# Kernel tuning notes

Measured on AMD Instinct MI355X. Metric: run time of the kernel, lower is better.

The kernel has to match this reference:

```python
import jax, jax.numpy as jnp
import numpy as np

N = 100000   # nodes
E = 1600000  # edges
F = 128      # in = out features
BN_EPS = 1e-5


def setup_inputs() -> dict:
    key = jax.random.key(0)
    ks = jax.random.split(key, 20)
    s = 1.0 / np.sqrt(F)
    inp = {
        "x": jax.random.normal(ks[0], (N, F), dtype=jnp.float32),
        "edge_index": jax.random.randint(ks[1], (2, E), 0, N, dtype=jnp.int64),
        "edge_type": jax.random.randint(ks[2], (E,), 0, 2, dtype=jnp.int64),
        # self-loop linear
        "w_sl": jax.random.normal(ks[3], (F, F), dtype=jnp.float32) * s,
        "b_sl": jnp.zeros((F,), dtype=jnp.float32),
        # GIN MLP for relation 0 (edge_type==0)
        "w1_n": jax.random.normal(ks[4], (F, F), dtype=jnp.float32) * s,
        "b1_n": jnp.zeros((F,), dtype=jnp.float32),
        "gamma_n": jnp.ones((F,), dtype=jnp.float32),
        "beta_n": jnp.zeros((F,), dtype=jnp.float32),
        "w2_n": jax.random.normal(ks[5], (F, F), dtype=jnp.float32) * s,
        "b2_n": jnp.zeros((F,), dtype=jnp.float32),
        # GIN MLP for relation 1 (edge_type==1)
        "w1_d": jax.random.normal(ks[6], (F, F), dtype=jnp.float32) * s,
        "b1_d": jnp.zeros((F,), dtype=jnp.float32),
        "gamma_d": jnp.ones((F,), dtype=jnp.float32),
        "beta_d": jnp.zeros((F,), dtype=jnp.float32),
        "w2_d": jax.random.normal(ks[7], (F, F), dtype=jnp.float32) * s,
        "b2_d": jnp.zeros((F,), dtype=jnp.float32),
        # gate linear: 3F -> F
        "w_gat": jax.random.normal(ks[8], (F, 3 * F), dtype=jnp.float32) * (1.0 / np.sqrt(3 * F)),
        "b_gat": jnp.zeros((F,), dtype=jnp.float32),
    }
    return inp


def _gin_branch(x, src, dst, mask, w1, b1, gamma, beta, w2, b2):
    # masked gather-scatter: equivalent to selecting edge columns with edge_type==r
    msg = x[src] * mask[:, None]                         # [E, F]
    agg = jax.ops.segment_sum(msg, dst, num_segments=N)  # [N, F]
    h = agg + x                                          # (1 + eps)*x with eps=0
    h = h @ w1.T + b1
    # BatchNorm1d, training-mode batch statistics (biased variance)
    mu = jnp.mean(h, axis=0)
    var = jnp.var(h, axis=0)
    h = gamma * (h - mu) * jax.lax.rsqrt(var + BN_EPS) + beta
    h = jax.nn.relu(h)
    return h @ w2.T + b2


def reference(x, edge_index, edge_type, w_sl, b_sl,
              w1_n, b1_n, gamma_n, beta_n, w2_n, b2_n,
              w1_d, b1_d, gamma_d, beta_d, w2_d, b2_d,
              w_gat, b_gat):
    src, dst = edge_index[0], edge_index[1]
    mask_n = (edge_type == 0).astype(x.dtype)
    mask_d = (edge_type == 1).astype(x.dtype)

    x_new_x = x @ w_sl.T + b_sl
    x_new_n = _gin_branch(x, src, dst, mask_n, w1_n, b1_n, gamma_n, beta_n, w2_n, b2_n)
    x_new_d = _gin_branch(x, src, dst, mask_d, w1_d, b1_d, gamma_d, beta_d, w2_d, b2_d)

    cat = jnp.concatenate((x_new_x, x_new_n, x_new_d), axis=1)   # [N, 3F]
    gat_raw = jax.nn.softmax(cat @ w_gat.T + b_gat, axis=-1)     # [N, F]
    gat = jnp.cumsum(gat_raw, axis=-1)
    out = (x_new_x + x_new_n) * (1.0 - gat) + (x_new_x + x_new_n + jnp.flip(x_new_d, axis=1)) * gat
    return out
```

## Files before the change

kernel.cpp:

```cpp
#include <hip/hip_runtime.h>
#include <stdint.h>

#define FF 128
#define MFMA __builtin_amdgcn_mfma_f32_16x16x32_bf16

typedef __attribute__((ext_vector_type(8))) short bf8_t;
typedef __attribute__((ext_vector_type(4))) float f4_t;
typedef __attribute__((ext_vector_type(8))) uint16_t us8_t;

__device__ __forceinline__ uint16_t f2bf(float f) {
  union { float f; uint32_t u; } v; v.f = f;
  return (uint16_t)((v.u + 0x7fffu + ((v.u >> 16) & 1u)) >> 16);
}
__device__ __forceinline__ float bf2f(uint16_t h) {
  union { uint32_t u; float f; } v; v.u = ((uint32_t)h) << 16;
  return v.f;
}

#define STAGE_W(Wp, rsb, cb)                                                   \
  do {                                                                         \
    uint4 tmp_[8];                                                             \
    _Pragma("unroll") for (int j_ = 0; j_ < 8; ++j_) {                         \
      int k_ = j_ * 4 + w;                                                     \
      int r_ = ((k_ & 1) << 6) + lane;                                         \
      int c_ = k_ >> 1;                                                        \
      tmp_[j_] = *(const uint4*)((const char*)(Wp) + (size_t)r_ * (rsb) +      \
                                 (cb) + c_ * 16);                              \
    }                                                                          \
    _Pragma("unroll") for (int j_ = 0; j_ < 8; ++j_) {                         \
      int k_ = j_ * 4 + w;                                                     \
      *(uint4*)((char*)wlds + k_ * 1024 + lane * 16) = tmp_[j_];               \
    }                                                                          \
  } while (0)

__global__ __launch_bounds__(256) void cvt_w_k(
    const float* __restrict__ wsl, const float* __restrict__ w1n,
    const float* __restrict__ w2n, const float* __restrict__ w1d,
    const float* __restrict__ w2d, const float* __restrict__ wgat,
    uint16_t* __restrict__ o) {
  int i = blockIdx.x * 256 + threadIdx.x;
  const int NW = 5 * 16384;
  if (i >= NW + 49152) return;
  float v;
  if (i < NW) {
    int wsel = i >> 14, j = i & 16383;
    const float* p = (wsel == 0) ? wsl : (wsel == 1) ? w1n : (wsel == 2) ? w2n
                     : (wsel == 3) ? w1d : w2d;
    v = p[j];
  } else {
    v = wgat[i - NW];
  }
  o[i] = f2bf(v);
}

__global__ __launch_bounds__(256) void cvt_x_k(const float* __restrict__ x,
                                               uint16_t* __restrict__ xb, int n4) {
  int i = blockIdx.x * 256 + threadIdx.x;
  if (i >= n4) return;
  float4 v = ((const float4*)x)[i];
  uint2 o;
  o.x = ((uint32_t)f2bf(v.y) << 16) | f2bf(v.x);
  o.y = ((uint32_t)f2bf(v.w) << 16) | f2bf(v.z);
  ((uint2*)xb)[i] = o;
}

__global__ __launch_bounds__(256) void hist_k(const int* __restrict__ dst,
                                              const int* __restrict__ ety,
                                              int* __restrict__ hist, int E) {
  int i = blockIdx.x * 256 + threadIdx.x;
  if (i < E) atomicAdd(&hist[(dst[i] << 1) | ety[i]], 1);
}

__global__ __launch_bounds__(256) void scan1_k(const int* __restrict__ hist,
                                               int* __restrict__ off,
                                               int* __restrict__ bsum, int nbins) {
  int i = blockIdx.x * 256 + threadIdx.x;
  int v = (i < nbins) ? hist[i] : 0;
  int lane = threadIdx.x & 63, w = threadIdx.x >> 6;
  int s = v;
#pragma unroll
  for (int d = 1; d < 64; d <<= 1) {
    int o = __shfl_up(s, (unsigned)d, 64);
    if (lane >= d) s += o;
  }
  __shared__ int wsum[4];
  if (lane == 63) wsum[w] = s;
  __syncthreads();
  int add = 0;
  for (int k = 0; k < w; ++k) add += wsum[k];
  s += add;
  if (i < nbins) off[i] = s - v;
  if (threadIdx.x == 255) bsum[blockIdx.x] = s;
}

__global__ __launch_bounds__(1024) void scan2_k(int* __restrict__ bsum, int nb) {
  int t = threadIdx.x;
  int v = (t < nb) ? bsum[t] : 0;
  int lane = t & 63, w = t >> 6;
  int s = v;
#pragma unroll
  for (int d = 1; d < 64; d <<= 1) {
    int o = __shfl_up(s, (unsigned)d, 64);
    if (lane >= d) s += o;
  }
  __shared__ int ws[16];
  if (lane == 63) ws[w] = s;
  __syncthreads();
  int add = 0;
  for (int k = 0; k < w; ++k) add += ws[k];
  s += add;
  if (t < nb) bsum[t] = s - v;
}

__global__ __launch_bounds__(256) void scan3_k(int* __restrict__ off,
                                               int* __restrict__ cur,
                                               const int* __restrict__ bsum,
                                               int nbins, int E) {
  int i = blockIdx.x * 256 + threadIdx.x;
  if (i < nbins) {
    int v = off[i] + bsum[blockIdx.x];
    off[i] = v;
    cur[i] = v;
  }
  if (i == nbins) off[i] = E;
}

__global__ __launch_bounds__(256) void sctidx_k(const int* __restrict__ src,
                                                const int* __restrict__ dst,
                                                const int* __restrict__ ety,
                                                int* __restrict__ cur,
                                                int* __restrict__ ssrc, int E) {
  int i = blockIdx.x * 256 + threadIdx.x;
  if (i < E) {
    int pos = atomicAdd(&cur[(dst[i] << 1) | ety[i]], 1);
    ssrc[pos] = src[i];
  }
}

__global__ __launch_bounds__(256) void agg_k(const int* __restrict__ off,
                                             const int* __restrict__ ssrc,
                                             const uint16_t* __restrict__ xb,
                                             const float* __restrict__ x,
                                             uint16_t* __restrict__ xanb,
                                             uint16_t* __restrict__ xadb, int nbins) {
  int wid = (blockIdx.x * 256 + threadIdx.x) >> 6;
  int lane = threadIdx.x & 63;
  if (wid >= nbins) return;
  int e = off[wid], end = off[wid + 1];
  float ax = 0.f, ay = 0.f, bx = 0.f, by = 0.f;
  for (; e + 7 < end; e += 8) {
    uint32_t v0 = ((const uint32_t*)(xb + (size_t)ssrc[e] * FF))[lane];
    uint32_t v1 = ((const uint32_t*)(xb + (size_t)ssrc[e + 1] * FF))[lane];
    uint32_t v2 = ((const uint32_t*)(xb + (size_t)ssrc[e + 2] * FF))[lane];
    uint32_t v3 = ((const uint32_t*)(xb + (size_t)ssrc[e + 3] * FF))[lane];
    uint32_t v4 = ((const uint32_t*)(xb + (size_t)ssrc[e + 4] * FF))[lane];
    uint32_t v5 = ((const uint32_t*)(xb + (size_t)ssrc[e + 5] * FF))[lane];
    uint32_t v6 = ((const uint32_t*)(xb + (size_t)ssrc[e + 6] * FF))[lane];
    uint32_t v7 = ((const uint32_t*)(xb + (size_t)ssrc[e + 7] * FF))[lane];
    ax += bf2f((uint16_t)(v0 & 0xffffu)) + bf2f((uint16_t)(v2 & 0xffffu)) +
          bf2f((uint16_t)(v4 & 0xffffu)) + bf2f((uint16_t)(v6 & 0xffffu));
    ay += bf2f((uint16_t)(v0 >> 16)) + bf2f((uint16_t)(v2 >> 16)) +
          bf2f((uint16_t)(v4 >> 16)) + bf2f((uint16_t)(v6 >> 16));
    bx += bf2f((uint16_t)(v1 & 0xffffu)) + bf2f((uint16_t)(v3 & 0xffffu)) +
          bf2f((uint16_t)(v5 & 0xffffu)) + bf2f((uint16_t)(v7 & 0xffffu));
    by += bf2f((uint16_t)(v1 >> 16)) + bf2f((uint16_t)(v3 >> 16)) +
          bf2f((uint16_t)(v5 >> 16)) + bf2f((uint16_t)(v7 >> 16));
  }
  for (; e + 1 < end; e += 2) {
    uint32_t v0 = ((const uint32_t*)(xb + (size_t)ssrc[e] * FF))[lane];
    uint32_t v1 = ((const uint32_t*)(xb + (size_t)ssrc[e + 1] * FF))[lane];
    ax += bf2f((uint16_t)(v0 & 0xffffu));
    ay += bf2f((uint16_t)(v0 >> 16));
    bx += bf2f((uint16_t)(v1 & 0xffffu));
    by += bf2f((uint16_t)(v1 >> 16));
  }
  if (e < end) {
    uint32_t v0 = ((const uint32_t*)(xb + (size_t)ssrc[e] * FF))[lane];
    ax += bf2f((uint16_t)(v0 & 0xffffu));
    ay += bf2f((uint16_t)(v0 >> 16));
  }
  ax += bx;
  ay += by;
  int n = wid >> 1;
  float2 xo = ((const float2*)(x + (size_t)n * FF))[lane];
  ax += xo.x;
  ay += xo.y;
  uint32_t o = ((uint32_t)f2bf(ay) << 16) | f2bf(ax);
  uint16_t* dstp = (wid & 1) ? xadb : xanb;
  ((uint32_t*)(dstp + (size_t)n * FF))[lane] = o;
}

__global__ __launch_bounds__(256) void gemm1_k(
    const uint16_t* __restrict__ xanb, const uint16_t* __restrict__ xadb,
    const uint16_t* __restrict__ wbf, const float* __restrict__ b1n,
    const float* __restrict__ b1d, uint16_t* __restrict__ h1n,
    uint16_t* __restrict__ h1d, float* __restrict__ gstats, int N) {
  __shared__ __align__(16) uint16_t wlds[16384];
  __shared__ float sstat[4][4][128];
  const int tid = threadIdx.x;
  const int lane = tid & 63, w = tid >> 6;
  const int lr = lane & 15, lg = lane >> 4;
  const int rowbase = blockIdx.x * 128 + w * 32;
  const int arow0 = min(rowbase + lr, N - 1);
  const int arow1 = min(rowbase + 16 + lr, N - 1);

  f4_t acc[2][8];
  const f4_t zz = {0.f, 0.f, 0.f, 0.f};
  bf8_t a0[4], a1[4];

  STAGE_W(wbf + 16384, 256, 0);
#pragma unroll
  for (int s = 0; s < 4; ++s) {
    const int k0 = s * 32 + lg * 8;
    a0[s] = *(const bf8_t*)(xanb + (size_t)arow0 * FF + k0);
    a1[s] = *(const bf8_t*)(xanb + (size_t)arow1 * FF + k0);
  }
  __syncthreads();

#pragma unroll 1
  for (int gi = 0; gi < 2; ++gi) {
#pragma unroll
    for (int rg = 0; rg < 2; ++rg)
#pragma unroll
      for (int t = 0; t < 8; ++t) acc[rg][t] = zz;
#pragma unroll
    for (int s = 0; s < 4; ++s) {
#pragma unroll
      for (int t = 0; t < 8; ++t) {
        bf8_t b = *(const bf8_t*)&wlds[(s * 4 + lg) * 1024 + (t * 16 + lr) * 8];
        acc[0][t] = MFMA(a0[s], b, acc[0][t], 0, 0, 0);
        acc[1][t] = MFMA(a1[s], b, acc[1][t], 0, 0, 0);
      }
    }
    const float* bp = gi ? b1d : b1n;
    uint16_t* hp = gi ? h1d : h1n;
#pragma unroll
    for (int t = 0; t < 8; ++t) {
      const int col = t * 16 + lr;
      const float b = bp[col];
      float sum = 0.f, ss = 0.f;
#pragma unroll
      for (int rg = 0; rg < 2; ++rg)
#pragma unroll
        for (int r = 0; r < 4; ++r) {
          const int row = rowbase + rg * 16 + lg * 4 + r;
          const float h = acc[rg][t][r] + b;
          if (row < N) {
            hp[(size_t)row * FF + col] = f2bf(h);
            sum += h;
            ss += h * h;
          }
        }
      sum += __shfl_xor(sum, 16, 64);
      sum += __shfl_xor(sum, 32, 64);
      ss += __shfl_xor(ss, 16, 64);
      ss += __shfl_xor(ss, 32, 64);
      if (lane < 16) {
        sstat[w][gi * 2 + 0][col] = sum;
        sstat[w][gi * 2 + 1][col] = ss;
      }
    }
    if (gi == 0) {
      __syncthreads();
      STAGE_W(wbf + 3 * 16384, 256, 0);
#pragma unroll
      for (int s = 0; s < 4; ++s) {
        const int k0 = s * 32 + lg * 8;
        a0[s] = *(const bf8_t*)(xadb + (size_t)arow0 * FF + k0);
        a1[s] = *(const bf8_t*)(xadb + (size_t)arow1 * FF + k0);
      }
      __syncthreads();
    }
  }
  __syncthreads();
  for (int i = tid; i < 512; i += 256) {
    int a = i >> 7, c = i & 127;
    float v = sstat[0][a][c] + sstat[1][a][c] + sstat[2][a][c] + sstat[3][a][c];
    unsafeAtomicAdd(&gstats[i], v);
  }
}

__global__ void bnfin_k(const float* __restrict__ gstats,
                        const float* __restrict__ gamn, const float* __restrict__ betn,
                        const float* __restrict__ gamd, const float* __restrict__ betd,
                        float* __restrict__ bnp, int N) {
  int i = threadIdx.x;
  float invN = 1.f / (float)N;
  {
    float mu = gstats[i] * invN;
    float var = gstats[128 + i] * invN - mu * mu;
    float sc = gamn[i] * rsqrtf(var + 1e-5f);
    bnp[i] = sc;
    bnp[128 + i] = betn[i] - mu * sc;
  }
  {
    float mu = gstats[256 + i] * invN;
    float var = gstats[384 + i] * invN - mu * mu;
    float sc = gamd[i] * rsqrtf(var + 1e-5f);
    bnp[256 + i] = sc;
    bnp[384 + i] = betd[i] - mu * sc;
  }
}

__global__ __launch_bounds__(256) void fuse2_k(
    const uint16_t* __restrict__ xb, const uint16_t* __restrict__ h1n,
    const uint16_t* __restrict__ h1d, const uint16_t* __restrict__ wbf,
    const float* __restrict__ bnp, const float* __restrict__ b_sl,
    const float* __restrict__ b2n, const float* __restrict__ b2d,
    const float* __restrict__ bgat, float* __restrict__ out, int N) {
  __shared__ __align__(16) uint16_t wlds[16384];
  __shared__ __align__(16) uint16_t smt[4][16][136];
  const int tid = threadIdx.x;
  const int lane = tid & 63, w = tid >> 6;
  const int lr = lane & 15, lg = lane >> 4;
  const int rowbase = blockIdx.x * 64 + w * 16;
  const int arow = min(rowbase + lr, N - 1);
  const uint16_t* wg = wbf + 5 * 16384;

  f4_t sum[8];
  f4_t accG[8];
  f4_t wk[8];
  const f4_t zz = {0.f, 0.f, 0.f, 0.f};

#define GATE_PHASE()                                                             \
  do {                                                                          \
    _Pragma("unroll") for (int s = 0; s < 4; ++s) {                             \
      bf8_t a = *(const bf8_t*)&smt[w][lr][s * 32 + lg * 8];                    \
      _Pragma("unroll") for (int t = 0; t < 8; ++t) {                           \
        bf8_t b = *(const bf8_t*)&wlds[(s * 4 + lg) * 1024 + (t * 16 + lr) * 8]; \
        accG[t] = MFMA(a, b, accG[t], 0, 0, 0);                                 \
      }                                                                         \
    }                                                                           \
  } while (0)

#define BRANCH_PHASE(hv, bnb, bp, ADDSUM)                                        \
  do {                                                                          \
    _Pragma("unroll") for (int t = 0; t < 8; ++t) wk[t] = zz;                   \
    _Pragma("unroll") for (int s = 0; s < 4; ++s) {                             \
      const int k0 = s * 32 + lg * 8;                                           \
      f4_t sc0 = *(const f4_t*)((bnb) + k0);                                    \
      f4_t sc1 = *(const f4_t*)((bnb) + k0 + 4);                                \
      f4_t sh0 = *(const f4_t*)((bnb) + 128 + k0);                              \
      f4_t sh1 = *(const f4_t*)((bnb) + 128 + k0 + 4);                          \
      bf8_t a;                                                                  \
      _Pragma("unroll") for (int j = 0; j < 4; ++j) {                           \
        a[j] = (short)f2bf(fmaxf(bf2f((hv)[s][j]) * sc0[j] + sh0[j], 0.f));     \
        a[j + 4] =                                                              \
            (short)f2bf(fmaxf(bf2f((hv)[s][j + 4]) * sc1[j] + sh1[j], 0.f));    \
      }                                                                         \
      _Pragma("unroll") for (int t = 0; t < 8; ++t) {                           \
        bf8_t b = *(const bf8_t*)&wlds[(s * 4 + lg) * 1024 + (t * 16 + lr) * 8]; \
        wk[t] = MFMA(a, b, wk[t], 0, 0, 0);                                     \
      }                                                                         \
    }                                                                           \
    _Pragma("unroll") for (int t = 0; t < 8; ++t) {                             \
      const int col = t * 16 + lr;                                              \
      const float bb = (bp)[col];                                               \
      _Pragma("unroll") for (int r = 0; r < 4; ++r) {                           \
        const float v = wk[t][r] + bb;                                          \
        if (ADDSUM) sum[t][r] += v;                                             \
        smt[w][lg * 4 + r][col] = f2bf(v);                                      \
      }                                                                         \
    }                                                                           \
  } while (0)

  bf8_t xa[4];
#pragma unroll
  for (int s = 0; s < 4; ++s)
    xa[s] = *(const bf8_t*)(xb + (size_t)arow * FF + s * 32 + lg * 8);

  STAGE_W(wbf, 256, 0);
  __syncthreads();

#pragma unroll
  for (int t = 0; t < 8; ++t) sum[t] = zz;
#pragma unroll
  for (int s = 0; s < 4; ++s) {
#pragma unroll
    for (int t = 0; t < 8; ++t) {
      bf8_t b = *(const bf8_t*)&wlds[(s * 4 + lg) * 1024 + (t * 16 + lr) * 8];
      sum[t] = MFMA(xa[s], b, sum[t], 0, 0, 0);
    }
  }
#pragma unroll
  for (int t = 0; t < 8; ++t) {
    const int col = t * 16 + lr;
    const float b = b_sl[col];
#pragma unroll
    for (int r = 0; r < 4; ++r) {
      sum[t][r] += b;
      smt[w][lg * 4 + r][col] = f2bf(sum[t][r]);
    }
  }
  us8_t hvn[4];
#pragma unroll
  for (int s = 0; s < 4; ++s)
    hvn[s] = *(const us8_t*)(h1n + (size_t)arow * FF + s * 32 + lg * 8);

  __syncthreads();
  STAGE_W(wg, 768, 0);
  __syncthreads();
#pragma unroll
  for (int t = 0; t < 8; ++t) accG[t] = zz;
  GATE_PHASE();

  __syncthreads();
  STAGE_W(wbf + 2 * 16384, 256, 0);
  __syncthreads();
  BRANCH_PHASE(hvn, bnp, b2n, 1);
  us8_t hvd[4];
#pragma unroll
  for (int s = 0; s < 4; ++s)
    hvd[s] = *(const us8_t*)(h1d + (size_t)arow * FF + s * 32 + lg * 8);

  __syncthreads();
  STAGE_W(wg, 768, 256);
  __syncthreads();
  GATE_PHASE();

  __syncthreads();
  STAGE_W(wbf + 4 * 16384, 256, 0);
  __syncthreads();
  BRANCH_PHASE(hvd, bnp + 256, b2d, 0);

  __syncthreads();
  STAGE_W(wg, 768, 512);
  __syncthreads();
  GATE_PHASE();

  float bg[8];
#pragma unroll
  for (int t = 0; t < 8; ++t) bg[t] = bgat[t * 16 + lr];
#pragma unroll
  for (int r = 0; r < 4; ++r) {
    float lv[8];
#pragma unroll
    for (int t = 0; t < 8; ++t) lv[t] = accG[t][r] + bg[t];
    float m = lv[0];
#pragma unroll
    for (int t = 1; t < 8; ++t) m = fmaxf(m, lv[t]);
#pragma unroll
    for (int d = 1; d < 16; d <<= 1) m = fmaxf(m, __shfl_xor(m, d, 16));
    float g[8];
    float run = 0.f;
#pragma unroll
    for (int t = 0; t < 8; ++t) {
      float p = __expf(lv[t] - m);
      float scn = p;
#pragma unroll
      for (int d = 1; d < 16; d <<= 1) {
        float o = __shfl_up(scn, (unsigned)d, 16);
        if (lr >= d) scn += o;
      }
      g[t] = run + scn;
      run += __shfl(scn, 15, 16);
    }
    const float inv = 1.f / run;
    const int row = rowbase + lg * 4 + r;
    if (row < N) {
      const int lrow = lg * 4 + r;
#pragma unroll
      for (int t = 0; t < 8; ++t) {
        const int col = t * 16 + lr;
        const float xdf = bf2f(smt[w][lrow][127 - col]);
        out[(size_t)row * FF + col] = sum[t][r] + xdf * (g[t] * inv);
      }
    }
  }
#undef GATE_PHASE
#undef BRANCH_PHASE
}

extern "C" void kernel_launch(void* const* d_in, const int* in_sizes, int n_in,
                              void* d_out, int out_size, void* d_ws, size_t ws_size,
                              hipStream_t stream) {
  const float* x = (const float*)d_in[0];
  const int* eidx = (const int*)d_in[1];
  const int* etype = (const int*)d_in[2];
  const float* w_sl = (const float*)d_in[3];
  const float* b_sl = (const float*)d_in[4];
  const float* w1n = (const float*)d_in[5];
  const float* b1n = (const float*)d_in[6];
  const float* gamn = (const float*)d_in[7];
  const float* betn = (const float*)d_in[8];
  const float* w2n = (const float*)d_in[9];
  const float* b2n = (const float*)d_in[10];
  const float* w1d = (const float*)d_in[11];
  const float* b1d = (const float*)d_in[12];
  const float* gamd = (const float*)d_in[13];
  const float* betd = (const float*)d_in[14];
  const float* w2d = (const float*)d_in[15];
  const float* b2d = (const float*)d_in[16];
  const float* wgat = (const float*)d_in[17];
  const float* bgat = (const float*)d_in[18];
  float* out = (float*)d_out;

  const int N = in_sizes[0] / FF;
  const int E = in_sizes[2];
  const int* src = eidx;
  const int* dst = eidx + E;
  const int nbins = 2 * N;

  const size_t NF = (size_t)N * FF;
  float* gstats = (float*)d_ws;
  float* bnp = gstats + 512;
  uint16_t* wbf = (uint16_t*)(bnp + 512);
  uint16_t* xb = wbf + 131072;
  uint16_t* xanb = xb + NF;
  uint16_t* xadb = xanb + NF;
  uint16_t* h1n = xadb + NF;
  uint16_t* h1d = h1n + NF;
  int* hist = (int*)(h1d + NF);
  int* off = hist + nbins;
  int* cur = off + nbins + 1;
  int* bsum = cur + nbins;
  int* ssrc = bsum + 1024;

  const int nb1 = (nbins + 255) / 256;

  hipMemsetAsync(hist, 0, (size_t)nbins * sizeof(int), stream);
  hipMemsetAsync(gstats, 0, 512 * sizeof(float), stream);
  cvt_w_k<<<512, 256, 0, stream>>>(w_sl, w1n, w2n, w1d, w2d, wgat, wbf);
  cvt_x_k<<<(int)((NF / 4 + 255) / 256), 256, 0, stream>>>(x, xb, (int)(NF / 4));

  hist_k<<<(E + 255) / 256, 256, 0, stream>>>(dst, etype, hist, E);
  scan1_k<<<nb1, 256, 0, stream>>>(hist, off, bsum, nbins);
  scan2_k<<<1, 1024, 0, stream>>>(bsum, nb1);
  scan3_k<<<(nbins + 256) / 256, 256, 0, stream>>>(off, cur, bsum, nbins, E);
  sctidx_k<<<(E + 255) / 256, 256, 0, stream>>>(src, dst, etype, cur, ssrc, E);
  agg_k<<<(nbins + 3) / 4, 256, 0, stream>>>(off, ssrc, xb, x, xanb, xadb, nbins);

  gemm1_k<<<(N + 127) / 128, 256, 0, stream>>>(xanb, xadb, wbf, b1n, b1d, h1n, h1d,
                                               gstats, N);
  bnfin_k<<<1, 128, 0, stream>>>(gstats, gamn, betn, gamd, betd, bnp, N);
  fuse2_k<<<(N + 63) / 64, 256, 0, stream>>>(xb, h1n, h1d, wbf, bnp, b_sl, b2n, b2d,
                                             bgat, out, N);
}
```

Baseline: 449.0 us.

## Replace per-bin atomic scatter with two-level bucketed counting sort

The CSR build now scatters edges first into coarse buckets of 512 bins with global atomics, packing the source id and local bin into one word. A second kernel then places each bucket's edges into exact positions using shared-memory atomics. This is meant to cut random global atomic traffic across 200k counters and make the scatter writes more local. The cost is an extra pass over the edges and an extra buffer. The packing also assumes source ids fit in 17 bits.

```diff
diff --git a/kernel.cpp b/kernel.cpp
--- a/kernel.cpp
+++ b/kernel.cpp
@@ -113,27 +113,46 @@
 }
 
 __global__ __launch_bounds__(256) void scan3_k(int* __restrict__ off,
-                                               int* __restrict__ cur,
+                                               int* __restrict__ ccur,
                                                const int* __restrict__ bsum,
                                                int nbins, int E) {
   int i = blockIdx.x * 256 + threadIdx.x;
   if (i < nbins) {
     int v = off[i] + bsum[blockIdx.x];
     off[i] = v;
-    cur[i] = v;
+    if ((i & 511) == 0) ccur[i >> 9] = v;
   }
   if (i == nbins) off[i] = E;
 }
 
-__global__ __launch_bounds__(256) void sctidx_k(const int* __restrict__ src,
-                                                const int* __restrict__ dst,
-                                                const int* __restrict__ ety,
-                                                int* __restrict__ cur,
-                                                int* __restrict__ ssrc, int E) {
+__global__ __launch_bounds__(256) void bucketize_k(const int* __restrict__ src,
+                                                   const int* __restrict__ dst,
+                                                   const int* __restrict__ ety,
+                                                   int* __restrict__ ccur,
+                                                   uint32_t* __restrict__ bk, int E) {
   int i = blockIdx.x * 256 + threadIdx.x;
   if (i < E) {
-    int pos = atomicAdd(&cur[(dst[i] << 1) | ety[i]], 1);
-    ssrc[pos] = src[i];
+    int bin = (dst[i] << 1) | ety[i];
+    int pos = atomicAdd(&ccur[bin >> 9], 1);
+    bk[pos] = (uint32_t)src[i] | ((uint32_t)(bin & 511) << 17);
+  }
+}
+
+__global__ __launch_bounds__(256) void sctfine_k(const int* __restrict__ off,
+                                                 const uint32_t* __restrict__ bk,
+                                                 int* __restrict__ ssrc, int nbins) {
+  __shared__ int lcur[512];
+  const int b = blockIdx.x;
+  const int binbase = b << 9;
+  const int binend = min(binbase + 512, nbins);
+  for (int j = threadIdx.x; j < binend - binbase; j += 256)
+    lcur[j] = off[binbase + j];
+  __syncthreads();
+  const int estart = off[binbase], eend = off[binend];
+  for (int i = estart + (int)threadIdx.x; i < eend; i += 256) {
+    uint32_t pk = bk[i];
+    int pos = atomicAdd(&lcur[pk >> 17], 1);
+    ssrc[pos] = (int)(pk & 0x1FFFFu);
   }
 }
 
@@ -500,6 +519,7 @@
   const int* src = eidx;
   const int* dst = eidx + E;
   const int nbins = 2 * N;
+  const int nbuckets = (nbins + 511) >> 9;
 
   const size_t NF = (size_t)N * FF;
   float* gstats = (float*)d_ws;
@@ -512,9 +532,10 @@
   uint16_t* h1d = h1n + NF;
   int* hist = (int*)(h1d + NF);
   int* off = hist + nbins;
-  int* cur = off + nbins + 1;
-  int* bsum = cur + nbins;
+  int* ccur = off + nbins + 1;
+  int* bsum = ccur + nbuckets;
   int* ssrc = bsum + 1024;
+  uint32_t* bk = (uint32_t*)(ssrc + E);
 
   const int nb1 = (nbins + 255) / 256;
 
@@ -526,8 +547,9 @@
   hist_k<<<(E + 255) / 256, 256, 0, stream>>>(dst, etype, hist, E);
   scan1_k<<<nb1, 256, 0, stream>>>(hist, off, bsum, nbins);
   scan2_k<<<1, 1024, 0, stream>>>(bsum, nb1);
-  scan3_k<<<(nbins + 256) / 256, 256, 0, stream>>>(off, cur, bsum, nbins, E);
-  sctidx_k<<<(E + 255) / 256, 256, 0, stream>>>(src, dst, etype, cur, ssrc, E);
+  scan3_k<<<(nbins + 256) / 256, 256, 0, stream>>>(off, ccur, bsum, nbins, E);
+  bucketize_k<<<(E + 255) / 256, 256, 0, stream>>>(src, dst, etype, ccur, bk, E);
+  sctfine_k<<<nbuckets, 256, 0, stream>>>(off, bk, ssrc, nbins);
   agg_k<<<(nbins + 3) / 4, 256, 0, stream>>>(off, ssrc, xb, x, xanb, xadb, nbins);
 
   gemm1_k<<<(N + 127) / 128, 256, 0, stream>>>(xanb, xadb, wbf, b1n, b1d, h1n, h1d,
```

New measurement: 909.9 us. +102.6%, slower.
